# Kernel optimization log

Hardware: AMD Instinct MI355X
Metric: run time of the kernel (lower is better)

## Reference

```python
import jax, jax.numpy as jnp
import numpy as np

T, B, D, H, Q = 512, 256, 256, 256, 256  # seq, batch, input_dim(=16^2), hidden_dim, n_qubits
CONV_THRESH = 0.0
GATE_THRESH = 0.5


def _parity_frac(bits):
    """Closed form of the RX({0,pi}) + CNOT-chain + measure circuit:
    final bit i is the prefix-XOR of thresholded input bits 0..i; the
    shot-averaged fraction of |1> outcomes is the mean of those parities.
    bits: (..., n_qubits) bool -> (...,) float32 in [0, 1]."""
    par = jnp.cumsum(bits.astype(jnp.float32), axis=-1) % 2.0
    return par.mean(axis=-1)


def setup_inputs() -> dict:
    key = jax.random.key(0)
    ks = jax.random.split(key, 9)
    s = 1.0 / np.sqrt(D + H)  # torch nn.Linear default init range
    def lin(kw, kb):
        W = jax.random.uniform(kw, (Q, D + H), jnp.float32, -s, s)
        b = jax.random.uniform(kb, (Q,), jnp.float32, -s, s)
        return W, b
    Wf, bf = lin(ks[1], ks[2])
    Wi, bi = lin(ks[3], ks[4])
    Wu, bu = lin(ks[5], ks[6])
    Wo, bo = lin(ks[7], ks[8])
    return {
        "inputs": jax.random.normal(ks[0], (T, B, D), jnp.float32),
        "hx0": jnp.zeros((B, H), jnp.float32),
        "cx0": jnp.zeros((B, H), jnp.float32),
        "Wf": Wf, "bf": bf, "Wi": Wi, "bi": bi,
        "Wu": Wu, "bu": bu, "Wo": Wo, "bo": bo,
    }


def reference(inputs, hx0, cx0, Wf, bf, Wi, bi, Wu, bu, Wo, bo):
    def step(carry, x):  # x: (B, D)
        hx, cx = carry
        # QuantumConv: deterministic parity fraction of thresholded pixels, per batch row
        conv = _parity_frac(x > CONV_THRESH)  # (B,)
        combined = jnp.concatenate(
            [x, jnp.broadcast_to(conv[:, None], (x.shape[0], hx.shape[1]))], axis=1
        )  # (B, D+H)
        def gate(W, b):
            raw = combined @ W.T + b  # (B, Q)
            return _parity_frac(raw > GATE_THRESH)[:, None]  # (B, 1)
        f = jax.nn.sigmoid(gate(Wf, bf))
        i = jax.nn.sigmoid(gate(Wi, bi))
        g = jnp.tanh(gate(Wu, bu))
        o = jax.nn.sigmoid(gate(Wo, bo))
        cx_new = f * cx + i * g
        hx_new = o * jnp.tanh(cx_new)
        return (hx_new, cx_new), hx_new

    (hx, cx), outs = jax.lax.scan(step, (hx0, cx0), inputs)
    return outs, hx, cx
```

## Files before the change

### kernel.cpp

```cpp
#include <hip/hip_runtime.h>
#include <math.h>

#define TT 512
#define BB 256
#define DD 256
#define HH 256
#define QQ 256
#define MM (TT*BB)
#define MTILE 16
#define WND 4e-4f
#define QCAP (1u<<19)

typedef float  f32x4  __attribute__((ext_vector_type(4)));
typedef short  bf16x8 __attribute__((ext_vector_type(8)));

__device__ __forceinline__ unsigned short bf16rn(float x){
    unsigned int u = __float_as_uint(x);
    unsigned int r = u + 0x7FFFu + ((u>>16)&1u);
    return (unsigned short)(r>>16);
}
__device__ __forceinline__ float bf2f(unsigned short h){
    return __uint_as_float(((unsigned int)h)<<16);
}

__global__ __launch_bounds__(256)
void prep_wc_k(const float* __restrict__ Wf, const float* __restrict__ Wi,
               const float* __restrict__ Wu, const float* __restrict__ Wo,
               const float* __restrict__ bf, const float* __restrict__ bi,
               const float* __restrict__ bu, const float* __restrict__ bo,
               float* __restrict__ wcf, float* __restrict__ ball)
{
    int n = blockIdx.x * 256 + threadIdx.x;
    int g = n >> 8, q = n & 255;
    const float* W    = (g==0) ? Wf : (g==1) ? Wi : (g==2) ? Wu : Wo;
    const float* bptr = (g==0) ? bf : (g==1) ? bi : (g==2) ? bu : bo;
    double s = 0.0;
    for (int j=0;j<256;j++) s += (double)W[q*512 + 256 + j];
    wcf[n] = (float)s; ball[n] = bptr[q];
}

__global__ __launch_bounds__(256)
void prep_bfrag_k(const float* __restrict__ Wf, const float* __restrict__ Wi,
                  const float* __restrict__ Wu, const float* __restrict__ Wo,
                  unsigned short* __restrict__ Bhi, unsigned short* __restrict__ Blo)
{
    int tau = blockIdx.x*256 + threadIdx.x;
    int kt = tau >> 12, rest = tau & 4095;
    int nt = rest >> 6, lane = rest & 63;
    int col = nt*16 + (lane & 15);
    int g = col >> 8, q = col & 255;
    const float* W = (g==0) ? Wf : (g==1) ? Wi : (g==2) ? Wu : Wo;
    int k0 = kt*32 + (lane>>4)*8;
    unsigned int hp[4], lp[4];
    #pragma unroll
    for (int jj=0;jj<4;jj++){
        float w0 = W[q*512 + k0 + 2*jj];
        float w1 = W[q*512 + k0 + 2*jj + 1];
        unsigned short h0 = bf16rn(w0), h1 = bf16rn(w1);
        unsigned short l0 = bf16rn(w0 - bf2f(h0)), l1 = bf16rn(w1 - bf2f(h1));
        hp[jj] = (unsigned int)h0 | ((unsigned int)h1 << 16);
        lp[jj] = (unsigned int)l0 | ((unsigned int)l1 << 16);
    }
    *(uint4*)(Bhi + (size_t)tau*8) = make_uint4(hp[0],hp[1],hp[2],hp[3]);
    *(uint4*)(Blo + (size_t)tau*8) = make_uint4(lp[0],lp[1],lp[2],lp[3]);
}

__global__ __launch_bounds__(256, 3)
void gates_k(const float* __restrict__ x,
             const unsigned short* __restrict__ Bhi, const unsigned short* __restrict__ Blo,
             const float* __restrict__ wcf, const float* __restrict__ ball,
             float* __restrict__ convbuf,
             unsigned long long* __restrict__ bits,
             unsigned int* __restrict__ qctr, unsigned int* __restrict__ qbuf)
{
    __shared__ unsigned short Ahi[MTILE*DD];
    __shared__ unsigned short Alo[MTILE*DD];
    __shared__ float convs[MTILE];
    const int tid = threadIdx.x;
    const int l   = tid & 63;
    const int w   = tid >> 6;
    const int m0  = blockIdx.x * MTILE;
    const unsigned long long ltm = (1ull<<l)-1ull;

    const float4* xin = (const float4*)(x + (size_t)m0 * DD);
    #pragma unroll
    for (int i=0;i<4;i++){
        int row = 4*i + w;
        float4 v = xin[256*i + tid];
        int b0=v.x>0.f, b1=v.y>0.f, b2=v.z>0.f, b3=v.w>0.f;
        int p1=b0^b1, p2=p1^b2, p3=p2^b3;
        int s=b0+p1+p2+p3;
        unsigned long long mask=__ballot(p3);
        int X=(int)(__popcll(mask&ltm)&1);
        int contrib = X ? 4-s : s;
        #pragma unroll
        for(int off=1;off<64;off<<=1) contrib += __shfl_xor(contrib,off);
        if (l==0){ float cv=(float)contrib*(1.0f/DD); convs[row]=cv; convbuf[m0+row]=cv; }
        unsigned short h0=bf16rn(v.x), h1=bf16rn(v.y), h2=bf16rn(v.z), h3=bf16rn(v.w);
        unsigned short q0=bf16rn(v.x-bf2f(h0)), q1=bf16rn(v.y-bf2f(h1));
        unsigned short q2=bf16rn(v.z-bf2f(h2)), q3=bf16rn(v.w-bf2f(h3));
        uint2 hi2 = make_uint2((unsigned)h0|((unsigned)h1<<16), (unsigned)h2|((unsigned)h3<<16));
        uint2 lo2 = make_uint2((unsigned)q0|((unsigned)q1<<16), (unsigned)q2|((unsigned)q3<<16));
        int baddr = (row*512 + l*8) ^ ((row&7)<<4);
        *(uint2*)((char*)Ahi + baddr) = hi2;
        *(uint2*)((char*)Alo + baddr) = lo2;
    }
    __syncthreads();

    f32x4 acc[16];
    #pragma unroll
    for (int t=0;t<16;t++) acc[t] = (f32x4){0.f,0.f,0.f,0.f};

    const int arow = l & 15;
    const int abase = arow*512 + (l>>4)*16;
    const int aswz = (arow&7)<<4;

    #pragma unroll
    for (int kt=0; kt<8; kt++){
        int aaddr = (abase + kt*64) ^ aswz;
        bf16x8 ah = *(const bf16x8*)((const char*)Ahi + aaddr);
        bf16x8 al = *(const bf16x8*)((const char*)Alo + aaddr);
        const unsigned short* bh = Bhi + ((size_t)(kt*64 + 16*w)*64 + l)*8;
        const unsigned short* bl = Blo + ((size_t)(kt*64 + 16*w)*64 + l)*8;
        #pragma unroll
        for (int t=0;t<16;t++){
            bf16x8 vbh = *(const bf16x8*)(bh + (size_t)t*512);
            bf16x8 vbl = *(const bf16x8*)(bl + (size_t)t*512);
            acc[t] = __builtin_amdgcn_mfma_f32_16x16x32_bf16(ah, vbh, acc[t], 0,0,0);
            acc[t] = __builtin_amdgcn_mfma_f32_16x16x32_bf16(ah, vbl, acc[t], 0,0,0);
            acc[t] = __builtin_amdgcn_mfma_f32_16x16x32_bf16(al, vbh, acc[t], 0,0,0);
        }
    }

    const int myu = l>>4, myj = l&3, mygrp = (l&15)>>2;
    float cva = convs[myu*4+0], cvb = convs[myu*4+1];
    float cvc = convs[myu*4+2], cvd = convs[myu*4+3];
    unsigned long long word = 0;
    #pragma unroll
    for (int t=0;t<16;t++){
        int n = w*256 + t*16 + (l&15);
        float wc = wcf[n], bb = ball[n];
        #pragma unroll
        for (int j=0;j<4;j++){
            float cj = (j==0)?cva:(j==1)?cvb:(j==2)?cvc:cvd;
            float rf = __fadd_rn(__fmaf_rn(cj, wc, acc[t][j]), bb);
            int bit = rf > 0.5f;
            unsigned long long B = __ballot(bit != 0);
            int cond = (j==myj) & ((t>>2)==myu);
            unsigned long long chunk = (B >> (mygrp*16)) & 0xFFFFull;
            word |= cond ? (chunk << ((t&3)*16)) : 0ull;
            bool win = fabsf(rf - 0.5f) < WND;
            unsigned long long wm = __ballot(win);
            if (wm){
                int leader = (int)__ffsll(wm) - 1;
                unsigned int cnt = (unsigned int)__popcll(wm);
                unsigned int base = 0;
                if (l == leader) base = atomicAdd(qctr, cnt);
                base = (unsigned int)__shfl((int)base, leader);
                if (win){
                    unsigned int pos = base + (unsigned int)__popcll(wm & ltm);
                    if (pos < QCAP){
                        unsigned int mrow = (unsigned int)(m0 + myu*4 + j);
                        qbuf[pos] = mrow | ((unsigned int)w<<17)
                                  | ((unsigned int)(t*16 + (l&15))<<19)
                                  | ((unsigned int)bit<<27);
                    }
                }
            }
        }
    }
    bits[((size_t)(m0 + arow)*4 + w)*4 + myu] = word;
}

__global__ __launch_bounds__(256)
void fixup_k(const float* __restrict__ x,
             const float* __restrict__ Wf, const float* __restrict__ Wi,
             const float* __restrict__ Wu, const float* __restrict__ Wo,
             const float* __restrict__ ball, const float* __restrict__ convbuf,
             const unsigned int* __restrict__ qctr, const unsigned int* __restrict__ qbuf,
             unsigned long long* __restrict__ bits)
{
    unsigned int cnt = *qctr; if (cnt > QCAP) cnt = QCAP;
    unsigned int stride = gridDim.x * blockDim.x;
    for (unsigned int i = blockIdx.x*blockDim.x + threadIdx.x; i < cnt; i += stride){
        unsigned int it = qbuf[i];
        int m = it & 0x1FFFF;
        int g = (it>>17)&3;
        int q = (it>>19)&255;
        int prov = (it>>27)&1;
        const float* W = (g==0)?Wf:(g==1)?Wi:(g==2)?Wu:Wo;
        const float* wr = W + (size_t)q*512;
        const float* xr = x + (size_t)m*DD;
        float cv = convbuf[m];
        float a = 0.f;
        for (int k=0;k<DD;k++) a = __fmaf_rn(xr[k], wr[k], a);
        for (int k=0;k<DD;k++) a = __fmaf_rn(cv, wr[DD+k], a);
        float raw = __fadd_rn(a, ball[g*256+q]);
        int bit = raw > 0.5f;
        if (bit != prov)
            atomicXor(&bits[((size_t)m*4 + g)*4 + (q>>6)], 1ull<<(q&63));
    }
}

__global__ __launch_bounds__(256)
void finalize_k(const unsigned long long* __restrict__ bits, float* __restrict__ gates)
{
    const int l = threadIdx.x & 63;
    const int wid = (int)((blockIdx.x*256 + threadIdx.x) >> 6);
    const unsigned long long ltm = (1ull<<l)-1ull;
    for (int it=0; it<32; it++){
        int R = wid*32 + it;
        unsigned long long wbits = bits[(size_t)R*4 + (l>>4)];
        int nib = (int)((wbits >> ((l&15)*4)) & 0xF);
        int b0=nib&1, b1=(nib>>1)&1, b2=(nib>>2)&1, b3=(nib>>3)&1;
        int p1=b0^b1, p2=p1^b2, p3=p2^b3;
        int s=b0+p1+p2+p3;
        unsigned long long mask=__ballot(p3);
        int X=(int)(__popcll(mask&ltm)&1);
        int contrib = X ? 4-s : s;
        #pragma unroll
        for(int off=1;off<64;off<<=1) contrib += __shfl_xor(contrib,off);
        if (l==0){
            int m = R>>2, g = R&3;
            float pf = (float)contrib*(1.0f/QQ);
            float val = (g==2) ? tanhf(pf) : 1.0f/(1.0f+expf(-pf));
            gates[(size_t)g*MM + m] = val;
        }
    }
}

__global__ __launch_bounds__(64)
void scan1_k(const float* __restrict__ gates, float* __restrict__ P,
             float* __restrict__ S)
{
    int b = blockIdx.x * 64 + threadIdx.x;
    const float* F = gates;
    const float* I = gates + MM;
    const float* G = gates + 2*(size_t)MM;
    float p = 1.f, s = 0.f;
    #pragma unroll 4
    for (int t=0;t<TT;t++){
        int m = t*BB + b;
        float f=F[m], i=I[m], g=G[m];
        s = __fadd_rn(__fmul_rn(f, s), __fmul_rn(i, g));
        p = __fmul_rn(p, f);
        P[m] = p; S[m] = s;
    }
}

__global__ __launch_bounds__(256)
void out_k(const float* __restrict__ gates, const float* __restrict__ P,
           const float* __restrict__ S, const float* __restrict__ cx0,
           float* __restrict__ out)
{
    int idx = blockIdx.x * 256 + threadIdx.x;
    int m  = idx >> 6;
    int h4 = (idx & 63) * 4;
    int b  = m & (BB-1);
    const float* O = gates + 3*(size_t)MM;
    float p = P[m], s = S[m], o = O[m];
    float4 c0 = *(const float4*)&cx0[b*HH + h4];
    float4 c, hv;
    c.x = __fadd_rn(__fmul_rn(p, c0.x), s);
    c.y = __fadd_rn(__fmul_rn(p, c0.y), s);
    c.z = __fadd_rn(__fmul_rn(p, c0.z), s);
    c.w = __fadd_rn(__fmul_rn(p, c0.w), s);
    hv.x = __fmul_rn(o, tanhf(c.x));
    hv.y = __fmul_rn(o, tanhf(c.y));
    hv.z = __fmul_rn(o, tanhf(c.z));
    hv.w = __fmul_rn(o, tanhf(c.w));
    *(float4*)&out[(size_t)m * HH + h4] = hv;
    if (m >= (TT-1)*BB){
        size_t base = (size_t)TT*BB*HH;
        *(float4*)&out[base + (size_t)b*HH + h4] = hv;
        *(float4*)&out[base + (size_t)BB*HH + (size_t)b*HH + h4] = c;
    }
}

extern "C" void kernel_launch(void* const* d_in, const int* in_sizes, int n_in,
                              void* d_out, int out_size, void* d_ws, size_t ws_size,
                              hipStream_t stream)
{
    const float* x   = (const float*)d_in[0];
    const float* cx0 = (const float*)d_in[2];
    const float* Wf  = (const float*)d_in[3];
    const float* bf  = (const float*)d_in[4];
    const float* Wi  = (const float*)d_in[5];
    const float* bi  = (const float*)d_in[6];
    const float* Wu  = (const float*)d_in[7];
    const float* bu  = (const float*)d_in[8];
    const float* Wo  = (const float*)d_in[9];
    const float* bo  = (const float*)d_in[10];

    char* ws = (char*)d_ws;
    unsigned short* Bhi   = (unsigned short*)(ws);
    unsigned short* Blo   = (unsigned short*)(ws + (512ul<<10));
    float* wcf            = (float*)(ws + (1ul<<20));
    float* ball           = (float*)(ws + (1ul<<20) + 4096);
    float* convbuf        = (float*)(ws + (1ul<<20) + 8192);
    float* gates          = (float*)(ws + (1ul<<20) + 8192 + (512ul<<10));
    char*  after_g        = ws + (1ul<<20) + 8192 + (512ul<<10) + (2ul<<20);
    float* Pbuf           = (float*)(after_g);
    float* Sbuf           = (float*)(after_g + (512ul<<10));
    unsigned int* qctr    = (unsigned int*)(after_g + (1ul<<20));
    unsigned int* qbuf    = (unsigned int*)(after_g + (1ul<<20) + 16);
    unsigned long long* bits = (unsigned long long*)d_out;
    float* out = (float*)d_out;

    hipMemsetAsync(qctr, 0, 4, stream);
    hipLaunchKernelGGL(prep_wc_k,    dim3(4),    dim3(256), 0, stream, Wf, Wi, Wu, Wo,
                       bf, bi, bu, bo, wcf, ball);
    hipLaunchKernelGGL(prep_bfrag_k, dim3(128),  dim3(256), 0, stream, Wf, Wi, Wu, Wo, Bhi, Blo);
    hipLaunchKernelGGL(gates_k,      dim3(MM/MTILE), dim3(256), 0, stream,
                       x, Bhi, Blo, wcf, ball, convbuf, bits, qctr, qbuf);
    hipLaunchKernelGGL(fixup_k,      dim3(256),  dim3(256), 0, stream,
                       x, Wf, Wi, Wu, Wo, ball, convbuf, qctr, qbuf, bits);
    hipLaunchKernelGGL(finalize_k,   dim3(4096), dim3(256), 0, stream, bits, gates);
    hipLaunchKernelGGL(scan1_k,      dim3(4),    dim3(64),  0, stream, gates, Pbuf, Sbuf);
    hipLaunchKernelGGL(out_k,        dim3((MM*HH/4)/256), dim3(256), 0, stream,
                       gates, Pbuf, Sbuf, cx0, out);
}
```

Baseline: 1.016 ms.

## Chunk the time recurrence scan and double the gate GEMM row tile

The sequential 512-step scan over 4 tiny blocks is split into a chunked three-phase scan: per-chunk local scans across 32 blocks, a short carry pass over chunk summaries, and the carry applied in the output kernel. The gate GEMM now handles 32 rows per block with two accumulator sets, so each loaded B fragment is reused twice, at the cost of more registers (launch bounds lowered to 2 waves). The fixup grid is also enlarged. Dropping explicit round-to-nearest intrinsics lets the compiler contract to FMA, which can slightly change numerics near the thresholds.

```diff
diff --git a/kernel.cpp b/kernel.cpp
--- a/kernel.cpp
+++ b/kernel.cpp
@@ -7,9 +7,11 @@
 #define HH 256
 #define QQ 256
 #define MM (TT*BB)
-#define MTILE 16
+#define MTILE 32
 #define WND 4e-4f
 #define QCAP (1u<<19)
+#define TCH 16
+#define NCH (TT/TCH)
 
 typedef float  f32x4  __attribute__((ext_vector_type(4)));
 typedef short  bf16x8 __attribute__((ext_vector_type(8)));
@@ -65,7 +67,7 @@
     *(uint4*)(Blo + (size_t)tau*8) = make_uint4(lp[0],lp[1],lp[2],lp[3]);
 }
 
-__global__ __launch_bounds__(256, 3)
+__global__ __launch_bounds__(256, 2)
 void gates_k(const float* __restrict__ x,
              const unsigned short* __restrict__ Bhi, const unsigned short* __restrict__ Blo,
              const float* __restrict__ wcf, const float* __restrict__ ball,
@@ -84,9 +86,9 @@
 
     const float4* xin = (const float4*)(x + (size_t)m0 * DD);
     #pragma unroll
-    for (int i=0;i<4;i++){
-        int row = 4*i + w;
-        float4 v = xin[256*i + tid];
+    for (int i=0;i<8;i++){
+        int row = 8*w + i;
+        float4 v = xin[row*64 + l];
         int b0=v.x>0.f, b1=v.y>0.f, b2=v.z>0.f, b3=v.w>0.f;
         int p1=b0^b1, p2=p1^b2, p3=p2^b3;
         int s=b0+p1+p2+p3;
@@ -107,69 +109,81 @@
     }
     __syncthreads();
 
-    f32x4 acc[16];
-    #pragma unroll
-    for (int t=0;t<16;t++) acc[t] = (f32x4){0.f,0.f,0.f,0.f};
-
-    const int arow = l & 15;
-    const int abase = arow*512 + (l>>4)*16;
-    const int aswz = (arow&7)<<4;
+    f32x4 acc0[16], acc1[16];
+    #pragma unroll
+    for (int t=0;t<16;t++){ acc0[t]=(f32x4){0,0,0,0}; acc1[t]=(f32x4){0,0,0,0}; }
+
+    const int r0  = l & 15;
+    const int ks  = l >> 4;
+    const int swz = (r0 & 7) << 4;
 
     #pragma unroll
     for (int kt=0; kt<8; kt++){
-        int aaddr = (abase + kt*64) ^ aswz;
-        bf16x8 ah = *(const bf16x8*)((const char*)Ahi + aaddr);
-        bf16x8 al = *(const bf16x8*)((const char*)Alo + aaddr);
+        int a0 = (r0*512 + ks*16 + kt*64) ^ swz;
+        int a1 = a0 + 16*512;
+        bf16x8 ah0 = *(const bf16x8*)((const char*)Ahi + a0);
+        bf16x8 al0 = *(const bf16x8*)((const char*)Alo + a0);
+        bf16x8 ah1 = *(const bf16x8*)((const char*)Ahi + a1);
+        bf16x8 al1 = *(const bf16x8*)((const char*)Alo + a1);
         const unsigned short* bh = Bhi + ((size_t)(kt*64 + 16*w)*64 + l)*8;
         const unsigned short* bl = Blo + ((size_t)(kt*64 + 16*w)*64 + l)*8;
         #pragma unroll
         for (int t=0;t<16;t++){
             bf16x8 vbh = *(const bf16x8*)(bh + (size_t)t*512);
             bf16x8 vbl = *(const bf16x8*)(bl + (size_t)t*512);
-            acc[t] = __builtin_amdgcn_mfma_f32_16x16x32_bf16(ah, vbh, acc[t], 0,0,0);
-            acc[t] = __builtin_amdgcn_mfma_f32_16x16x32_bf16(ah, vbl, acc[t], 0,0,0);
-            acc[t] = __builtin_amdgcn_mfma_f32_16x16x32_bf16(al, vbh, acc[t], 0,0,0);
+            acc0[t] = __builtin_amdgcn_mfma_f32_16x16x32_bf16(ah0, vbh, acc0[t], 0,0,0);
+            acc0[t] = __builtin_amdgcn_mfma_f32_16x16x32_bf16(al0, vbh, acc0[t], 0,0,0);
+            acc0[t] = __builtin_amdgcn_mfma_f32_16x16x32_bf16(ah0, vbl, acc0[t], 0,0,0);
+            acc1[t] = __builtin_amdgcn_mfma_f32_16x16x32_bf16(ah1, vbh, acc1[t], 0,0,0);
+            acc1[t] = __builtin_amdgcn_mfma_f32_16x16x32_bf16(al1, vbh, acc1[t], 0,0,0);
+            acc1[t] = __builtin_amdgcn_mfma_f32_16x16x32_bf16(ah1, vbl, acc1[t], 0,0,0);
         }
     }
 
     const int myu = l>>4, myj = l&3, mygrp = (l&15)>>2;
-    float cva = convs[myu*4+0], cvb = convs[myu*4+1];
-    float cvc = convs[myu*4+2], cvd = convs[myu*4+3];
-    unsigned long long word = 0;
-    #pragma unroll
-    for (int t=0;t<16;t++){
-        int n = w*256 + t*16 + (l&15);
-        float wc = wcf[n], bb = ball[n];
-        #pragma unroll
-        for (int j=0;j<4;j++){
-            float cj = (j==0)?cva:(j==1)?cvb:(j==2)?cvc:cvd;
-            float rf = __fadd_rn(__fmaf_rn(cj, wc, acc[t][j]), bb);
-            int bit = rf > 0.5f;
-            unsigned long long B = __ballot(bit != 0);
-            int cond = (j==myj) & ((t>>2)==myu);
-            unsigned long long chunk = (B >> (mygrp*16)) & 0xFFFFull;
-            word |= cond ? (chunk << ((t&3)*16)) : 0ull;
-            bool win = fabsf(rf - 0.5f) < WND;
-            unsigned long long wm = __ballot(win);
-            if (wm){
-                int leader = (int)__ffsll(wm) - 1;
-                unsigned int cnt = (unsigned int)__popcll(wm);
-                unsigned int base = 0;
-                if (l == leader) base = atomicAdd(qctr, cnt);
-                base = (unsigned int)__shfl((int)base, leader);
-                if (win){
-                    unsigned int pos = base + (unsigned int)__popcll(wm & ltm);
-                    if (pos < QCAP){
-                        unsigned int mrow = (unsigned int)(m0 + myu*4 + j);
-                        qbuf[pos] = mrow | ((unsigned int)w<<17)
-                                  | ((unsigned int)(t*16 + (l&15))<<19)
-                                  | ((unsigned int)bit<<27);
-                    }
-                }
-            }
-        }
-    }
-    bits[((size_t)(m0 + arow)*4 + w)*4 + myu] = word;
+
+#define EPILOGUE(ACC, M2)                                                          \
+    {                                                                              \
+        unsigned long long word = 0;                                               \
+        _Pragma("unroll")                                                          \
+        for (int t=0;t<16;t++){                                                    \
+            int n = w*256 + t*16 + (l&15);                                         \
+            float wc = wcf[n], bb = ball[n];                                       \
+            _Pragma("unroll")                                                      \
+            for (int j=0;j<4;j++){                                                 \
+                float cj = convs[(M2)*16 + myu*4 + j];                             \
+                float rf = __fadd_rn(__fmaf_rn(cj, wc, ACC[t][j]), bb);            \
+                int bit = rf > 0.5f;                                               \
+                unsigned long long B = __ballot(bit != 0);                         \
+                int cond = (j==myj) & ((t>>2)==myu);                               \
+                unsigned long long chunk = (B >> (mygrp*16)) & 0xFFFFull;          \
+                word |= cond ? (chunk << ((t&3)*16)) : 0ull;                       \
+                bool win = fabsf(rf - 0.5f) < WND;                                 \
+                unsigned long long wm = __ballot(win);                             \
+                if (wm){                                                           \
+                    int leader = (int)__ffsll(wm) - 1;                             \
+                    unsigned int cnt = (unsigned int)__popcll(wm);                 \
+                    unsigned int base = 0;                                         \
+                    if (l == leader) base = atomicAdd(qctr, cnt);                  \
+                    base = (unsigned int)__shfl((int)base, leader);                \
+                    if (win){                                                      \
+                        unsigned int pos = base + (unsigned int)__popcll(wm & ltm);\
+                        if (pos < QCAP){                                           \
+                            unsigned int mrow = (unsigned int)(m0 + (M2)*16 + myu*4 + j); \
+                            qbuf[pos] = mrow | ((unsigned int)w<<17)               \
+                                      | ((unsigned int)(t*16 + (l&15))<<19)        \
+                                      | ((unsigned int)bit<<27);                   \
+                        }                                                          \
+                    }                                                              \
+                }                                                                  \
+            }                                                                      \
+        }                                                                          \
+        bits[((size_t)(m0 + (M2)*16 + r0)*4 + w)*4 + myu] = word;                  \
+    }
+
+    EPILOGUE(acc0, 0)
+    EPILOGUE(acc1, 1)
+#undef EPILOGUE
 }
 
 __global__ __launch_bounds__(256)
@@ -229,46 +243,65 @@
     }
 }
 
-__global__ __launch_bounds__(64)
-void scan1_k(const float* __restrict__ gates, float* __restrict__ P,
-             float* __restrict__ S)
-{
-    int b = blockIdx.x * 64 + threadIdx.x;
+__global__ __launch_bounds__(256)
+void scanA_k(const float* __restrict__ gates, float* __restrict__ P,
+             float* __restrict__ S, float* __restrict__ Psum, float* __restrict__ Ssum)
+{
+    int b  = threadIdx.x;
+    int ch = blockIdx.x;
     const float* F = gates;
     const float* I = gates + MM;
     const float* G = gates + 2*(size_t)MM;
     float p = 1.f, s = 0.f;
-    #pragma unroll 4
-    for (int t=0;t<TT;t++){
-        int m = t*BB + b;
+    #pragma unroll
+    for (int tt=0;tt<TCH;tt++){
+        int m = (ch*TCH + tt)*BB + b;
         float f=F[m], i=I[m], g=G[m];
-        s = __fadd_rn(__fmul_rn(f, s), __fmul_rn(i, g));
-        p = __fmul_rn(p, f);
+        s = f*s + i*g;
+        p = p*f;
         P[m] = p; S[m] = s;
     }
+    Psum[ch*BB + b] = p; Ssum[ch*BB + b] = s;
+}
+
+__global__ __launch_bounds__(256)
+void scanB_k(const float* __restrict__ Psum, const float* __restrict__ Ssum,
+             float* __restrict__ Ppre, float* __restrict__ Spre)
+{
+    int b = threadIdx.x;
+    float cp = 1.f, cs = 0.f;
+    for (int ch=0; ch<NCH; ch++){
+        Ppre[ch*BB + b] = cp; Spre[ch*BB + b] = cs;
+        float p = Psum[ch*BB + b], s = Ssum[ch*BB + b];
+        cs = p*cs + s;
+        cp = cp*p;
+    }
 }
 
 __global__ __launch_bounds__(256)
 void out_k(const float* __restrict__ gates, const float* __restrict__ P,
-           const float* __restrict__ S, const float* __restrict__ cx0,
+           const float* __restrict__ S, const float* __restrict__ Ppre,
+           const float* __restrict__ Spre, const float* __restrict__ cx0,
            float* __restrict__ out)
 {
     int idx = blockIdx.x * 256 + threadIdx.x;
     int m  = idx >> 6;
     int h4 = (idx & 63) * 4;
     int b  = m & (BB-1);
+    int ch = m >> 12;
     const float* O = gates + 3*(size_t)MM;
     float p = P[m], s = S[m], o = O[m];
+    float pp = Ppre[ch*BB + b], ss = Spre[ch*BB + b];
     float4 c0 = *(const float4*)&cx0[b*HH + h4];
     float4 c, hv;
-    c.x = __fadd_rn(__fmul_rn(p, c0.x), s);
-    c.y = __fadd_rn(__fmul_rn(p, c0.y), s);
-    c.z = __fadd_rn(__fmul_rn(p, c0.z), s);
-    c.w = __fadd_rn(__fmul_rn(p, c0.w), s);
-    hv.x = __fmul_rn(o, tanhf(c.x));
-    hv.y = __fmul_rn(o, tanhf(c.y));
-    hv.z = __fmul_rn(o, tanhf(c.z));
-    hv.w = __fmul_rn(o, tanhf(c.w));
+    c.x = p*(pp*c0.x + ss) + s;
+    c.y = p*(pp*c0.y + ss) + s;
+    c.z = p*(pp*c0.z + ss) + s;
+    c.w = p*(pp*c0.w + ss) + s;
+    hv.x = o*tanhf(c.x);
+    hv.y = o*tanhf(c.y);
+    hv.z = o*tanhf(c.z);
+    hv.w = o*tanhf(c.w);
     *(float4*)&out[(size_t)m * HH + h4] = hv;
     if (m >= (TT-1)*BB){
         size_t base = (size_t)TT*BB*HH;
@@ -293,17 +326,20 @@
     const float* bo  = (const float*)d_in[10];
 
     char* ws = (char*)d_ws;
-    unsigned short* Bhi   = (unsigned short*)(ws);
-    unsigned short* Blo   = (unsigned short*)(ws + (512ul<<10));
-    float* wcf            = (float*)(ws + (1ul<<20));
-    float* ball           = (float*)(ws + (1ul<<20) + 4096);
-    float* convbuf        = (float*)(ws + (1ul<<20) + 8192);
-    float* gates          = (float*)(ws + (1ul<<20) + 8192 + (512ul<<10));
-    char*  after_g        = ws + (1ul<<20) + 8192 + (512ul<<10) + (2ul<<20);
-    float* Pbuf           = (float*)(after_g);
-    float* Sbuf           = (float*)(after_g + (512ul<<10));
-    unsigned int* qctr    = (unsigned int*)(after_g + (1ul<<20));
-    unsigned int* qbuf    = (unsigned int*)(after_g + (1ul<<20) + 16);
+    unsigned short* Bhi = (unsigned short*)(ws);
+    unsigned short* Blo = (unsigned short*)(ws + 0x080000);
+    float* wcf     = (float*)(ws + 0x100000);
+    float* ball    = (float*)(ws + 0x101000);
+    float* convbuf = (float*)(ws + 0x104000);
+    float* gates   = (float*)(ws + 0x184000);
+    float* Pbuf    = (float*)(ws + 0x384000);
+    float* Sbuf    = (float*)(ws + 0x404000);
+    float* Psum    = (float*)(ws + 0x484000);
+    float* Ssum    = (float*)(ws + 0x48C000);
+    float* Ppre    = (float*)(ws + 0x494000);
+    float* Spre    = (float*)(ws + 0x49C000);
+    unsigned int* qctr = (unsigned int*)(ws + 0x4A4000);
+    unsigned int* qbuf = (unsigned int*)(ws + 0x4A4100);
     unsigned long long* bits = (unsigned long long*)d_out;
     float* out = (float*)d_out;
 
@@ -313,10 +349,11 @@
     hipLaunchKernelGGL(prep_bfrag_k, dim3(128),  dim3(256), 0, stream, Wf, Wi, Wu, Wo, Bhi, Blo);
     hipLaunchKernelGGL(gates_k,      dim3(MM/MTILE), dim3(256), 0, stream,
                        x, Bhi, Blo, wcf, ball, convbuf, bits, qctr, qbuf);
-    hipLaunchKernelGGL(fixup_k,      dim3(256),  dim3(256), 0, stream,
+    hipLaunchKernelGGL(fixup_k,      dim3(1024), dim3(256), 0, stream,
                        x, Wf, Wi, Wu, Wo, ball, convbuf, qctr, qbuf, bits);
     hipLaunchKernelGGL(finalize_k,   dim3(4096), dim3(256), 0, stream, bits, gates);
-    hipLaunchKernelGGL(scan1_k,      dim3(4),    dim3(64),  0, stream, gates, Pbuf, Sbuf);
+    hipLaunchKernelGGL(scanA_k,      dim3(NCH),  dim3(256), 0, stream, gates, Pbuf, Sbuf, Psum, Ssum);
+    hipLaunchKernelGGL(scanB_k,      dim3(1),    dim3(256), 0, stream, Psum, Ssum, Ppre, Spre);
     hipLaunchKernelGGL(out_k,        dim3((MM*HH/4)/256), dim3(256), 0, stream,
-                       gates, Pbuf, Sbuf, cx0, out);
-}
+                       gates, Pbuf, Sbuf, Ppre, Spre, cx0, out);
+}
```

After: 976.4 us. 1.04x faster.
